# Kernel tuning notes

Measured on AMD Instinct MI355X. Metric: run time of the kernel, lower is better.

## Reference

```python
import jax, jax.numpy as jnp
import numpy as np

N, BS, DIM, SIZE = 512, 64, 256, 8192

def setup_inputs() -> dict:
    key = jax.random.key(0)
    k1, k2 = jax.random.split(key)
    seq = jax.random.normal(k1, (N, BS, DIM), dtype=jnp.float32)
    # codebook initialized Uniform[-1, 1] as in _reset_parameters
    vocab = jax.random.uniform(k2, (SIZE, DIM), dtype=jnp.float32, minval=-1.0, maxval=1.0)
    return {"seq": seq, "vocab": vocab}

def reference(seq, vocab):
    n, bs, d = seq.shape
    x = seq.reshape(n * bs, d)                                   # [T, D]
    # squared euclidean distances; argmin identical to cdist(p=2).argmin
    x2 = jnp.sum(x * x, axis=-1, keepdims=True)                  # [T, 1]
    v2 = jnp.sum(vocab * vocab, axis=-1)                         # [K]
    d2 = x2 - 2.0 * (x @ vocab.T) + v2                           # [T, K]
    ingredients = jnp.argmin(d2, axis=1)                          # [T]
    out = jnp.take(vocab, ingredients, axis=0).reshape(n, bs, d)  # quantized seq
    return out, ingredients.reshape(n, bs)
```

## Files before the change

### kernel.cpp

```cpp
#include <hip/hip_runtime.h>

#define T_TOTAL 32768
#define D       256
#define K       8192
#define BQ      64
#define KSPLIT  4
#define KSLICE  (K / KSPLIT)
#define NSLICE  (KSPLIT * 4)
#define NCT     (K / 16)
#define KT_STRIDE (NCT * 64 * 8)
#define NQB     (T_TOTAL / BQ)

typedef _Float16 half4f  __attribute__((ext_vector_type(4)));
typedef _Float16 half8f  __attribute__((ext_vector_type(8)));
typedef float    floatx4 __attribute__((ext_vector_type(4)));

#define PARTIAL_F 1048576
#define BHALVES   2097152

__global__ void hv2_kernel(const float* __restrict__ vocab, float* __restrict__ hv2) {
    int code = blockIdx.x * 4 + (threadIdx.x >> 6);
    int lane = threadIdx.x & 63;
    const float4* row = (const float4*)(vocab + (size_t)code * D);
    float4 v = row[lane];
    float s = v.x * v.x + v.y * v.y + v.z * v.z + v.w * v.w;
    #pragma unroll
    for (int off = 32; off; off >>= 1) s += __shfl_down(s, off, 64);
    if (lane == 0) hv2[code] = 0.5f * s;
}

__device__ __forceinline__ _Float16 hi16(float x) { return (_Float16)x; }
__device__ __forceinline__ _Float16 lo16(float x, _Float16 h) { return (_Float16)(x - (float)h); }
__device__ __forceinline__ void split4(float4 v, half4f& h, half4f& l) {
    _Float16 hx = hi16(v.x), hy = hi16(v.y), hz = hi16(v.z), hw = hi16(v.w);
    h = (half4f){hx, hy, hz, hw};
    l = (half4f){lo16(v.x, hx), lo16(v.y, hy), lo16(v.z, hz), lo16(v.w, hw)};
}

__global__ void bsplit_kernel(const float* __restrict__ vocab,
                              _Float16* __restrict__ bhi, _Float16* __restrict__ blo) {
    const int ct = blockIdx.x;
    const int t  = threadIdx.x;
    const int k4 = t & 63;
    const float4* voc4 = (const float4*)vocab;
    const int kt = k4 >> 3, kg = (k4 >> 1) & 3, h = k4 & 1;
    #pragma unroll
    for (int ci = 0; ci < 4; ++ci) {
        int cc = (t >> 6) * 4 + ci;
        float4 v = voc4[(size_t)(ct * 16 + cc) * (D / 4) + k4];
        half4f hh, ll;
        split4(v, hh, ll);
        size_t off = (((size_t)kt * NCT + ct) * 64 + (cc + 16 * kg)) * 8 + h * 4;
        *(half4f*)&bhi[off] = hh;
        *(half4f*)&blo[off] = ll;
    }
}

__launch_bounds__(256, 2)
__global__ void argmin_kernel(const float* __restrict__ seq,
                              const _Float16* __restrict__ bhi,
                              const _Float16* __restrict__ blo,
                              const float* __restrict__ hv2,
                              float2* __restrict__ partial) {
    __shared__ _Float16 AhL[4 * 8 * 64 * 8];
    __shared__ _Float16 AlL[4 * 8 * 64 * 8];

    const int t    = threadIdx.x;
    const int lane = t & 63;
    const int wn   = t >> 6;
    const int bi   = blockIdx.x;
    const int slice = (bi & 7) >> 1;
    const int qb    = (bi >> 3) * 2 + (bi & 1);
    const int q0   = qb * BQ;
    const int k0   = slice * KSLICE;

    const float4* seq4 = (const float4*)seq;

    #pragma unroll
    for (int i = 0; i < 16; ++i) {
        int f   = t + 256 * i;
        int row = f >> 6;
        int d4  = f & 63;
        float4 v = seq4[(size_t)(q0 + row) * (D / 4) + d4];
        half4f h, l;
        split4(v, h, l);
        int kt = d4 >> 3, kg = (d4 >> 1) & 3, hh = d4 & 1;
        int off = (((((row >> 4) * 8 + kt) * 64) + ((row & 15) + 16 * kg)) * 8 + hh * 4)
                  ^ (kt << 3);
        *(half4f*)&AhL[off] = h;
        *(half4f*)&AlL[off] = l;
    }
    __syncthreads();

    float best[16];
    int   bidx[16];
    #pragma unroll
    for (int b = 0; b < 16; ++b) { best[b] = 3.4e38f; bidx[b] = 0; }

    const _Float16* bh_l = bhi + (size_t)lane * 8;
    const _Float16* bl_l = blo + (size_t)lane * 8;

    for (int c0i = 0; c0i < KSLICE / 256; ++c0i) {
        const int c0  = k0 + c0i * 256;
        const int ct0 = (c0 >> 4) + wn * 4;
        const size_t cb = (size_t)ct0 * 512;

        floatx4 acc[4][4];
        #pragma unroll
        for (int mi = 0; mi < 4; ++mi)
            #pragma unroll
            for (int nj = 0; nj < 4; ++nj) acc[mi][nj] = (floatx4){0.f, 0.f, 0.f, 0.f};

        half8f bh0[4], bl0[4], bh1[4], bl1[4];
        #pragma unroll
        for (int nj = 0; nj < 4; ++nj) {
            bh0[nj] = *(const half8f*)&bh_l[cb + nj * 512];
            bl0[nj] = *(const half8f*)&bl_l[cb + nj * 512];
        }

        #pragma unroll 1
        for (int kt2 = 0; kt2 < 4; ++kt2) {
            const int kt = kt2 * 2;
            {
                const size_t kb = (size_t)(kt + 1) * KT_STRIDE + cb;
                #pragma unroll
                for (int nj = 0; nj < 4; ++nj) {
                    bh1[nj] = *(const half8f*)&bh_l[kb + nj * 512];
                    bl1[nj] = *(const half8f*)&bl_l[kb + nj * 512];
                }
            }
            {
                half8f ah[4], al[4];
                #pragma unroll
                for (int mi = 0; mi < 4; ++mi) {
                    const int ao = (((mi * 8 + kt) * 64 + lane) * 8) ^ (kt << 3);
                    ah[mi] = *(const half8f*)&AhL[ao];
                    al[mi] = *(const half8f*)&AlL[ao];
                }
                #pragma unroll
                for (int nj = 0; nj < 4; ++nj)
                    #pragma unroll
                    for (int mi = 0; mi < 4; ++mi) {
                        floatx4 a = acc[mi][nj];
                        a = __builtin_amdgcn_mfma_f32_16x16x32_f16(al[mi], bh0[nj], a, 0, 0, 0);
                        a = __builtin_amdgcn_mfma_f32_16x16x32_f16(ah[mi], bl0[nj], a, 0, 0, 0);
                        a = __builtin_amdgcn_mfma_f32_16x16x32_f16(ah[mi], bh0[nj], a, 0, 0, 0);
                        acc[mi][nj] = a;
                    }
            }
            if (kt2 < 3) {
                const size_t kb = (size_t)(kt + 2) * KT_STRIDE + cb;
                #pragma unroll
                for (int nj = 0; nj < 4; ++nj) {
                    bh0[nj] = *(const half8f*)&bh_l[kb + nj * 512];
                    bl0[nj] = *(const half8f*)&bl_l[kb + nj * 512];
                }
            }
            {
                half8f ah[4], al[4];
                #pragma unroll
                for (int mi = 0; mi < 4; ++mi) {
                    const int ao = (((mi * 8 + kt + 1) * 64 + lane) * 8) ^ ((kt + 1) << 3);
                    ah[mi] = *(const half8f*)&AhL[ao];
                    al[mi] = *(const half8f*)&AlL[ao];
                }
                #pragma unroll
                for (int nj = 0; nj < 4; ++nj)
                    #pragma unroll
                    for (int mi = 0; mi < 4; ++mi) {
                        floatx4 a = acc[mi][nj];
                        a = __builtin_amdgcn_mfma_f32_16x16x32_f16(al[mi], bh1[nj], a, 0, 0, 0);
                        a = __builtin_amdgcn_mfma_f32_16x16x32_f16(ah[mi], bl1[nj], a, 0, 0, 0);
                        a = __builtin_amdgcn_mfma_f32_16x16x32_f16(ah[mi], bh1[nj], a, 0, 0, 0);
                        acc[mi][nj] = a;
                    }
            }
        }

        #pragma unroll
        for (int nj = 0; nj < 4; ++nj) {
            int c = c0 + (wn * 4 + nj) * 16 + (lane & 15);
            float hv = hv2[c];
            #pragma unroll
            for (int mi = 0; mi < 4; ++mi)
                #pragma unroll
                for (int r = 0; r < 4; ++r) {
                    float s = hv - acc[mi][nj][r];
                    int b = mi * 4 + r;
                    if (s < best[b]) { best[b] = s; bidx[b] = c; }
                }
        }
    }

    #pragma unroll
    for (int off = 1; off < 16; off <<= 1) {
        #pragma unroll
        for (int b = 0; b < 16; ++b) {
            float ob = __shfl_xor(best[b], off, 64);
            int   oi = __shfl_xor(bidx[b], off, 64);
            if (ob < best[b] || (ob == best[b] && oi < bidx[b])) {
                best[b] = ob; bidx[b] = oi;
            }
        }
    }
    if ((lane & 15) == 0) {
        const size_t sl = (size_t)(slice * 4 + wn) * T_TOTAL;
        #pragma unroll
        for (int mi = 0; mi < 4; ++mi)
            #pragma unroll
            for (int r = 0; r < 4; ++r) {
                int q = q0 + mi * 16 + (lane >> 4) * 4 + r;
                partial[sl + q] = make_float2(best[mi * 4 + r], (float)bidx[mi * 4 + r]);
            }
    }
}

__global__ void reduce_kernel(const float2* __restrict__ partial, int* __restrict__ idx) {
    int q = blockIdx.x * 256 + threadIdx.x;
    float bm = 3.4e38f;
    int   bi = 0x7fffffff;
    #pragma unroll
    for (int s = 0; s < NSLICE; ++s) {
        float2 p = partial[(size_t)s * T_TOTAL + q];
        int pi = (int)p.y;
        if (p.x < bm || (p.x == bm && pi < bi)) { bm = p.x; bi = pi; }
    }
    idx[q] = bi;
}

__global__ void gather_kernel(const float* __restrict__ vocab,
                              const int* __restrict__ idx,
                              float* __restrict__ out) {
    int r    = blockIdx.x * 4 + (threadIdx.x >> 6);
    int lane = threadIdx.x & 63;
    int k = idx[r];
    const float4* src = (const float4*)(vocab + (size_t)k * D);
    float4*       dst = (float4*)(out + (size_t)r * D);
    dst[lane] = src[lane];
    if (lane == 0) out[(size_t)T_TOTAL * D + r] = (float)k;
}

extern "C" void kernel_launch(void* const* d_in, const int* in_sizes, int n_in,
                              void* d_out, int out_size, void* d_ws, size_t ws_size,
                              hipStream_t stream) {
    const float* seq   = (const float*)d_in[0];
    const float* vocab = (const float*)d_in[1];
    float* out = (float*)d_out;

    float* hv2 = (float*)d_ws;
    int*   idx = (int*)((char*)d_ws + K * sizeof(float));

    float2*   partial = (float2*)d_out;
    _Float16* bhi = (_Float16*)(out + PARTIAL_F);
    _Float16* blo = bhi + BHALVES;

    hipLaunchKernelGGL(hv2_kernel,    dim3(K / 4),           dim3(256), 0, stream, vocab, hv2);
    hipLaunchKernelGGL(bsplit_kernel, dim3(NCT),             dim3(256), 0, stream, vocab, bhi, blo);
    hipLaunchKernelGGL(argmin_kernel, dim3(NQB * KSPLIT),    dim3(256), 0, stream,
                       seq, bhi, blo, hv2, partial);
    hipLaunchKernelGGL(reduce_kernel, dim3(T_TOTAL / 256),   dim3(256), 0, stream, partial, idx);
    hipLaunchKernelGGL(gather_kernel, dim3(T_TOTAL / 4),     dim3(256), 0, stream, vocab, idx, out);
}
```

Measured before the change: 445.9 us.

## Fuse prep kernels, prefetch A fragments, and merge reduce with gather

Merges the hv2 norm computation into the vocab split kernel so the vocab is read once. The argmin inner loop now double-buffers the LDS A fragments alongside the B fragments, loading the next k-step before issuing MFMAs to hide LDS latency. It also adds a fused reduce+gather kernel that keeps partials in workspace, when the workspace is large enough, so partial results are not written into the output buffer. This removes two launches and the idx round trip, at the cost of more registers in the argmin loop.

```diff
diff --git a/kernel.cpp b/kernel.cpp
--- a/kernel.cpp
+++ b/kernel.cpp
@@ -18,17 +18,6 @@
 #define PARTIAL_F 1048576
 #define BHALVES   2097152
 
-__global__ void hv2_kernel(const float* __restrict__ vocab, float* __restrict__ hv2) {
-    int code = blockIdx.x * 4 + (threadIdx.x >> 6);
-    int lane = threadIdx.x & 63;
-    const float4* row = (const float4*)(vocab + (size_t)code * D);
-    float4 v = row[lane];
-    float s = v.x * v.x + v.y * v.y + v.z * v.z + v.w * v.w;
-    #pragma unroll
-    for (int off = 32; off; off >>= 1) s += __shfl_down(s, off, 64);
-    if (lane == 0) hv2[code] = 0.5f * s;
-}
-
 __device__ __forceinline__ _Float16 hi16(float x) { return (_Float16)x; }
 __device__ __forceinline__ _Float16 lo16(float x, _Float16 h) { return (_Float16)(x - (float)h); }
 __device__ __forceinline__ void split4(float4 v, half4f& h, half4f& l) {
@@ -37,22 +26,33 @@
     l = (half4f){lo16(v.x, hx), lo16(v.y, hy), lo16(v.z, hz), lo16(v.w, hw)};
 }
 
-__global__ void bsplit_kernel(const float* __restrict__ vocab,
-                              _Float16* __restrict__ bhi, _Float16* __restrict__ blo) {
+__global__ void prep_kernel(const float* __restrict__ vocab,
+                            _Float16* __restrict__ bhi, _Float16* __restrict__ blo,
+                            float* __restrict__ hv2) {
     const int ct = blockIdx.x;
     const int t  = threadIdx.x;
     const int k4 = t & 63;
+    const int w  = t >> 6;
     const float4* voc4 = (const float4*)vocab;
     const int kt = k4 >> 3, kg = (k4 >> 1) & 3, h = k4 & 1;
+    float ss[4];
     #pragma unroll
     for (int ci = 0; ci < 4; ++ci) {
-        int cc = (t >> 6) * 4 + ci;
+        int cc = w * 4 + ci;
         float4 v = voc4[(size_t)(ct * 16 + cc) * (D / 4) + k4];
         half4f hh, ll;
         split4(v, hh, ll);
         size_t off = (((size_t)kt * NCT + ct) * 64 + (cc + 16 * kg)) * 8 + h * 4;
         *(half4f*)&bhi[off] = hh;
         *(half4f*)&blo[off] = ll;
+        ss[ci] = v.x * v.x + v.y * v.y + v.z * v.z + v.w * v.w;
+    }
+    #pragma unroll
+    for (int ci = 0; ci < 4; ++ci) {
+        float s = ss[ci];
+        #pragma unroll
+        for (int off = 32; off; off >>= 1) s += __shfl_down(s, off, 64);
+        if ((t & 63) == 0) hv2[ct * 16 + w * 4 + ci] = 0.5f * s;
     }
 }
 
@@ -112,10 +112,17 @@
             for (int nj = 0; nj < 4; ++nj) acc[mi][nj] = (floatx4){0.f, 0.f, 0.f, 0.f};
 
         half8f bh0[4], bl0[4], bh1[4], bl1[4];
+        half8f ah0[4], al0[4], ah1[4], al1[4];
         #pragma unroll
         for (int nj = 0; nj < 4; ++nj) {
             bh0[nj] = *(const half8f*)&bh_l[cb + nj * 512];
             bl0[nj] = *(const half8f*)&bl_l[cb + nj * 512];
+        }
+        #pragma unroll
+        for (int mi = 0; mi < 4; ++mi) {
+            const int ao = ((mi * 8) * 64 + lane) * 8;
+            ah0[mi] = *(const half8f*)&AhL[ao];
+            al0[mi] = *(const half8f*)&AlL[ao];
         }
 
         #pragma unroll 1
@@ -128,26 +135,23 @@
                     bh1[nj] = *(const half8f*)&bh_l[kb + nj * 512];
                     bl1[nj] = *(const half8f*)&bl_l[kb + nj * 512];
                 }
-            }
-            {
-                half8f ah[4], al[4];
-                #pragma unroll
-                for (int mi = 0; mi < 4; ++mi) {
-                    const int ao = (((mi * 8 + kt) * 64 + lane) * 8) ^ (kt << 3);
-                    ah[mi] = *(const half8f*)&AhL[ao];
-                    al[mi] = *(const half8f*)&AlL[ao];
-                }
-                #pragma unroll
-                for (int nj = 0; nj < 4; ++nj)
-                    #pragma unroll
-                    for (int mi = 0; mi < 4; ++mi) {
-                        floatx4 a = acc[mi][nj];
-                        a = __builtin_amdgcn_mfma_f32_16x16x32_f16(al[mi], bh0[nj], a, 0, 0, 0);
-                        a = __builtin_amdgcn_mfma_f32_16x16x32_f16(ah[mi], bl0[nj], a, 0, 0, 0);
-                        a = __builtin_amdgcn_mfma_f32_16x16x32_f16(ah[mi], bh0[nj], a, 0, 0, 0);
-                        acc[mi][nj] = a;
-                    }
-            }
+                #pragma unroll
+                for (int mi = 0; mi < 4; ++mi) {
+                    const int ao = (((mi * 8 + kt + 1) * 64 + lane) * 8) ^ ((kt + 1) << 3);
+                    ah1[mi] = *(const half8f*)&AhL[ao];
+                    al1[mi] = *(const half8f*)&AlL[ao];
+                }
+            }
+            #pragma unroll
+            for (int nj = 0; nj < 4; ++nj)
+                #pragma unroll
+                for (int mi = 0; mi < 4; ++mi) {
+                    floatx4 a = acc[mi][nj];
+                    a = __builtin_amdgcn_mfma_f32_16x16x32_f16(al0[mi], bh0[nj], a, 0, 0, 0);
+                    a = __builtin_amdgcn_mfma_f32_16x16x32_f16(ah0[mi], bl0[nj], a, 0, 0, 0);
+                    a = __builtin_amdgcn_mfma_f32_16x16x32_f16(ah0[mi], bh0[nj], a, 0, 0, 0);
+                    acc[mi][nj] = a;
+                }
             if (kt2 < 3) {
                 const size_t kb = (size_t)(kt + 2) * KT_STRIDE + cb;
                 #pragma unroll
@@ -155,26 +159,23 @@
                     bh0[nj] = *(const half8f*)&bh_l[kb + nj * 512];
                     bl0[nj] = *(const half8f*)&bl_l[kb + nj * 512];
                 }
-            }
-            {
-                half8f ah[4], al[4];
-                #pragma unroll
-                for (int mi = 0; mi < 4; ++mi) {
-                    const int ao = (((mi * 8 + kt + 1) * 64 + lane) * 8) ^ ((kt + 1) << 3);
-                    ah[mi] = *(const half8f*)&AhL[ao];
-                    al[mi] = *(const half8f*)&AlL[ao];
-                }
-                #pragma unroll
-                for (int nj = 0; nj < 4; ++nj)
-                    #pragma unroll
-                    for (int mi = 0; mi < 4; ++mi) {
-                        floatx4 a = acc[mi][nj];
-                        a = __builtin_amdgcn_mfma_f32_16x16x32_f16(al[mi], bh1[nj], a, 0, 0, 0);
-                        a = __builtin_amdgcn_mfma_f32_16x16x32_f16(ah[mi], bl1[nj], a, 0, 0, 0);
-                        a = __builtin_amdgcn_mfma_f32_16x16x32_f16(ah[mi], bh1[nj], a, 0, 0, 0);
-                        acc[mi][nj] = a;
-                    }
-            }
+                #pragma unroll
+                for (int mi = 0; mi < 4; ++mi) {
+                    const int ao = (((mi * 8 + kt + 2) * 64 + lane) * 8) ^ ((kt + 2) << 3);
+                    ah0[mi] = *(const half8f*)&AhL[ao];
+                    al0[mi] = *(const half8f*)&AlL[ao];
+                }
+            }
+            #pragma unroll
+            for (int nj = 0; nj < 4; ++nj)
+                #pragma unroll
+                for (int mi = 0; mi < 4; ++mi) {
+                    floatx4 a = acc[mi][nj];
+                    a = __builtin_amdgcn_mfma_f32_16x16x32_f16(al1[mi], bh1[nj], a, 0, 0, 0);
+                    a = __builtin_amdgcn_mfma_f32_16x16x32_f16(ah1[mi], bl1[nj], a, 0, 0, 0);
+                    a = __builtin_amdgcn_mfma_f32_16x16x32_f16(ah1[mi], bh1[nj], a, 0, 0, 0);
+                    acc[mi][nj] = a;
+                }
         }
 
         #pragma unroll
@@ -213,6 +214,30 @@
                 partial[sl + q] = make_float2(best[mi * 4 + r], (float)bidx[mi * 4 + r]);
             }
     }
+}
+
+__global__ void redgather_kernel(const float* __restrict__ vocab,
+                                 const float2* __restrict__ partial,
+                                 float* __restrict__ out) {
+    int r    = blockIdx.x * 4 + (threadIdx.x >> 6);
+    int lane = threadIdx.x & 63;
+    float bm = 3.4e38f;
+    int   bi = 0x7fffffff;
+    if (lane < 16) {
+        float2 p = partial[(size_t)lane * T_TOTAL + r];
+        bm = p.x; bi = (int)p.y;
+    }
+    #pragma unroll
+    for (int off = 1; off < 16; off <<= 1) {
+        float ob = __shfl_xor(bm, off, 64);
+        int   oi = __shfl_xor(bi, off, 64);
+        if (ob < bm || (ob == bm && oi < bi)) { bm = ob; bi = oi; }
+    }
+    int k = __shfl(bi, 0, 64);
+    const float4* src = (const float4*)(vocab + (size_t)k * D);
+    float4*       dst = (float4*)(out + (size_t)r * D);
+    dst[lane] = src[lane];
+    if (lane == 0) out[(size_t)T_TOTAL * D + r] = (float)k;
 }
 
 __global__ void reduce_kernel(const float2* __restrict__ partial, int* __restrict__ idx) {
@@ -248,16 +273,26 @@
     float* out = (float*)d_out;
 
     float* hv2 = (float*)d_ws;
-    int*   idx = (int*)((char*)d_ws + K * sizeof(float));
-
-    float2*   partial = (float2*)d_out;
     _Float16* bhi = (_Float16*)(out + PARTIAL_F);
     _Float16* blo = bhi + BHALVES;
 
-    hipLaunchKernelGGL(hv2_kernel,    dim3(K / 4),           dim3(256), 0, stream, vocab, hv2);
-    hipLaunchKernelGGL(bsplit_kernel, dim3(NCT),             dim3(256), 0, stream, vocab, bhi, blo);
-    hipLaunchKernelGGL(argmin_kernel, dim3(NQB * KSPLIT),    dim3(256), 0, stream,
-                       seq, bhi, blo, hv2, partial);
-    hipLaunchKernelGGL(reduce_kernel, dim3(T_TOTAL / 256),   dim3(256), 0, stream, partial, idx);
-    hipLaunchKernelGGL(gather_kernel, dim3(T_TOTAL / 4),     dim3(256), 0, stream, vocab, idx, out);
-}
+    const size_t need_ws = (size_t)(K + 2 * NSLICE * T_TOTAL) * sizeof(float) + 256;
+    const bool fused = ws_size >= need_ws;
+
+    hipLaunchKernelGGL(prep_kernel, dim3(NCT), dim3(256), 0, stream, vocab, bhi, blo, hv2);
+
+    if (fused) {
+        float2* partial = (float2*)(hv2 + K);
+        hipLaunchKernelGGL(argmin_kernel,    dim3(NQB * KSPLIT), dim3(256), 0, stream,
+                           seq, bhi, blo, hv2, partial);
+        hipLaunchKernelGGL(redgather_kernel, dim3(T_TOTAL / 4),  dim3(256), 0, stream,
+                           vocab, partial, out);
+    } else {
+        float2* partial = (float2*)d_out;
+        int* idx = (int*)(hv2 + K);
+        hipLaunchKernelGGL(argmin_kernel, dim3(NQB * KSPLIT), dim3(256), 0, stream,
+                           seq, bhi, blo, hv2, partial);
+        hipLaunchKernelGGL(reduce_kernel, dim3(T_TOTAL / 256), dim3(256), 0, stream, partial, idx);
+        hipLaunchKernelGGL(gather_kernel, dim3(T_TOTAL / 4),   dim3(256), 0, stream, vocab, idx, out);
+    }
+}
```

After: 434.2 us. 1.03x faster.
